# Optimization experiments

Hardware: AMD Instinct MI355X
Metric: run time of the kernel (lower is better)

Reference implementation:

```python
import jax, jax.numpy as jnp
import numpy as np

N_NODES = 100000
N_EDGES = 1600000
IN_DIM = 128
HEADS = 4
OUT_DIM = 32
NEG_SLOPE = 0.2  # PyG GATConv default negative_slope


def setup_inputs() -> dict:
    key = jax.random.key(0)
    k_x, k_e, k_w, k_as, k_ad = jax.random.split(key, 5)
    x = jax.random.normal(k_x, (N_NODES, IN_DIM), dtype=jnp.float32)
    edge_index = jax.random.randint(k_e, (2, N_EDGES), 0, N_NODES, dtype=jnp.int64)
    # Glorot-style init for learned parameters (GATConv lin + attention vectors)
    W = jax.random.normal(k_w, (IN_DIM, HEADS * OUT_DIM), dtype=jnp.float32) / np.sqrt(IN_DIM)
    att_src = jax.random.normal(k_as, (HEADS, OUT_DIM), dtype=jnp.float32) / np.sqrt(OUT_DIM)
    att_dst = jax.random.normal(k_ad, (HEADS, OUT_DIM), dtype=jnp.float32) / np.sqrt(OUT_DIM)
    bias = jnp.zeros((HEADS * OUT_DIM,), dtype=jnp.float32)
    return {"x": x, "edge_index": edge_index, "W": W, "att_src": att_src,
            "att_dst": att_dst, "bias": bias}


def reference(x, edge_index, W, att_src, att_dst, bias):
    N = x.shape[0]
    H, D = att_src.shape
    # PyG GATConv default: add self loops
    loop = jnp.arange(N, dtype=edge_index.dtype)
    src = jnp.concatenate([edge_index[0], loop])  # message sources  [E+N]
    dst = jnp.concatenate([edge_index[1], loop])  # message targets  [E+N]

    h = (x @ W).reshape(N, H, D)                          # [N, H, D]
    a_src = jnp.einsum('nhd,hd->nh', h, att_src)          # [N, H]
    a_dst = jnp.einsum('nhd,hd->nh', h, att_dst)          # [N, H]

    # per-edge attention logits, LeakyReLU(neg_slope=0.2)
    e = jax.nn.leaky_relu(a_src[src] + a_dst[dst], NEG_SLOPE)  # [E+N, H]

    # segment softmax over edges grouped by target node (numerically stable)
    e_max = jax.ops.segment_max(e, dst, num_segments=N)        # [N, H]
    e_max = jnp.where(jnp.isfinite(e_max), e_max, jnp.float32(0))
    ex = jnp.exp(e - e_max[dst])                               # [E+N, H]
    denom = jax.ops.segment_sum(ex, dst, num_segments=N)       # [N, H]
    alpha = ex / (denom[dst] + jnp.float32(1e-16))             # [E+N, H]

    # weighted scatter-aggregate of source features
    msg = h[src] * alpha[:, :, None]                           # [E+N, H, D]
    out = jax.ops.segment_sum(msg, dst, num_segments=N)        # [N, H, D]
    out = out.reshape(N, H * D) + bias                         # concat heads + bias
    return jax.nn.elu(out)                                     # wrapper ELU
```

## Files before the change

kernel.cpp:

```cpp
#include <hip/hip_runtime.h>
#include <hip/hip_fp16.h>
#include <math.h>

#define N_NODES 100000
#define N_EDGES 1600000
#define IN_DIM 128
#define F_DIM 128
#define NEG_SLOPE 0.2f

#define BUCKW_LOG 7
#define NBUCK 784
#define NBLK 128
#define EPB 12500
#define G_TOT (NBUCK * NBLK)
#define SC_CHUNK 4096
#define SC_NB ((G_TOT + SC_CHUNK - 1) / SC_CHUNK)
#define CSR_CAP (N_EDGES + NBUCK * 384)

typedef short v8s __attribute__((ext_vector_type(8)));
typedef float v4f __attribute__((ext_vector_type(4)));

static __device__ __forceinline__ unsigned short f2bf(float f) {
    unsigned u = __float_as_uint(f);
    u += 0x7fffu + ((u >> 16) & 1u);
    return (unsigned short)(u >> 16);
}
static __device__ __forceinline__ float bf2f(unsigned s) { return __uint_as_float(s << 16); }
static __device__ __forceinline__ float lo2f(unsigned u) { return __uint_as_float(u << 16); }
static __device__ __forceinline__ float hi2f(unsigned u) { return __uint_as_float(u & 0xffff0000u); }

__global__ __launch_bounds__(256) void k_wprep(const float* __restrict__ W,
                                               unsigned short* __restrict__ Wt) {
    int i = blockIdx.x * 256 + threadIdx.x;
    int n = i >> 7, k = i & 127;
    Wt[n * 128 + k] = f2bf(W[k * 128 + n]);
}

__global__ __launch_bounds__(256) void k_gemm(const float* __restrict__ x,
                                              const unsigned short* __restrict__ Wt,
                                              unsigned short* __restrict__ h16,
                                              const float* __restrict__ att_src,
                                              const float* __restrict__ att_dst,
                                              float* __restrict__ a_src,
                                              float* __restrict__ a_dst) {
    __shared__ unsigned short As[64][136];
    __shared__ unsigned short Bs[128][136];
    __shared__ float attl[256];
    const int t  = threadIdx.x;
    const int n0 = blockIdx.x * 64;

    attl[t] = (t < 128) ? att_src[t] : att_dst[t - 128];

    {
        int row = t >> 2, k0 = (t & 3) * 32;
        int n = n0 + row;
        #pragma unroll
        for (int i = 0; i < 4; i++) {
            float4 va = make_float4(0.f,0.f,0.f,0.f), vb = va;
            if (n < N_NODES) {
                const float* p = x + (size_t)n * IN_DIM + k0 + i * 8;
                va = *(const float4*)p;
                vb = *(const float4*)(p + 4);
            }
            uint4 u;
            u.x = f2bf(va.x) | ((unsigned)f2bf(va.y) << 16);
            u.y = f2bf(va.z) | ((unsigned)f2bf(va.w) << 16);
            u.z = f2bf(vb.x) | ((unsigned)f2bf(vb.y) << 16);
            u.w = f2bf(vb.z) | ((unsigned)f2bf(vb.w) << 16);
            *(uint4*)&As[row][k0 + i * 8] = u;
        }
    }
    {
        int nr = t >> 1, s0 = (t & 1) * 64;
        const uint4* src = (const uint4*)(Wt + nr * 128 + s0);
        #pragma unroll
        for (int i = 0; i < 8; i++)
            *(uint4*)&Bs[nr][s0 + i * 8] = src[i];
    }
    __syncthreads();

    const int w = t >> 6, lane = t & 63;
    const int mr = lane & 15, quad = lane >> 4;
    const int m0 = w * 16;

    v4f acc[8];
    #pragma unroll
    for (int nt = 0; nt < 8; nt++) acc[nt] = (v4f){0.f, 0.f, 0.f, 0.f};

    #pragma unroll
    for (int kk = 0; kk < 4; kk++) {
        int kof = kk * 32 + quad * 8;
        v8s a = *(const v8s*)&As[m0 + mr][kof];
        #pragma unroll
        for (int nt = 0; nt < 8; nt++) {
            v8s b = *(const v8s*)&Bs[nt * 16 + mr][kof];
            acc[nt] = __builtin_amdgcn_mfma_f32_16x16x32_bf16(a, b, acc[nt], 0, 0, 0);
        }
    }

    #pragma unroll
    for (int nt = 0; nt < 8; nt++)
        #pragma unroll
        for (int r = 0; r < 4; r++)
            As[m0 + quad * 4 + r][nt * 16 + mr] = f2bf(acc[nt][r]);
    __syncthreads();
    {
        int row = m0 + (lane >> 2);
        int c0  = (lane & 3) * 32;
        int n = n0 + row;
        if (n < N_NODES) {
            float ds = 0.f, dd = 0.f;
            #pragma unroll
            for (int i = 0; i < 4; i++) {
                uint4 v = *(const uint4*)&As[row][c0 + i * 8];
                *(uint4*)&h16[(size_t)n * F_DIM + c0 + i * 8] = v;
                float f0 = lo2f(v.x), f1 = hi2f(v.x);
                float f2 = lo2f(v.y), f3 = hi2f(v.y);
                float f4 = lo2f(v.z), f5 = hi2f(v.z);
                float f6 = lo2f(v.w), f7 = hi2f(v.w);
                const float* ps = &attl[c0 + i * 8];
                const float* pd = &attl[128 + c0 + i * 8];
                ds += f0*ps[0] + f1*ps[1] + f2*ps[2] + f3*ps[3]
                    + f4*ps[4] + f5*ps[5] + f6*ps[6] + f7*ps[7];
                dd += f0*pd[0] + f1*pd[1] + f2*pd[2] + f3*pd[3]
                    + f4*pd[4] + f5*pd[5] + f6*pd[6] + f7*pd[7];
            }
            int hd = lane & 3;
            a_src[n * 4 + hd] = ds;
            a_dst[n * 4 + hd] = dd;
        }
    }
}

__global__ __launch_bounds__(1024) void k_bhist(const int* __restrict__ ei_dst,
                                                int* __restrict__ G) {
    __shared__ int hist[NBUCK];
    for (int i = threadIdx.x; i < NBUCK; i += 1024) hist[i] = 0;
    __syncthreads();
    const int4* p = (const int4*)(ei_dst + blockIdx.x * EPB);
    const int n4 = EPB / 4;
    for (int i = threadIdx.x; i < n4; i += 1024) {
        int4 d = p[i];
        atomicAdd(&hist[d.x >> BUCKW_LOG], 1);
        atomicAdd(&hist[d.y >> BUCKW_LOG], 1);
        atomicAdd(&hist[d.z >> BUCKW_LOG], 1);
        atomicAdd(&hist[d.w >> BUCKW_LOG], 1);
    }
    __syncthreads();
    for (int b = threadIdx.x; b < NBUCK; b += 1024)
        G[b * NBLK + blockIdx.x] = hist[b];
}

__global__ __launch_bounds__(256) void k_scanp(const int* __restrict__ a,
                                               int* __restrict__ part) {
    int base = blockIdx.x * SC_CHUNK + threadIdx.x * 16;
    int s = 0;
    #pragma unroll
    for (int i = 0; i < 16; i++) {
        int idx = base + i;
        if (idx < G_TOT) s += a[idx];
    }
    __shared__ int wsum[4];
    for (int off = 32; off >= 1; off >>= 1) s += __shfl_down(s, off, 64);
    if ((threadIdx.x & 63) == 0) wsum[threadIdx.x >> 6] = s;
    __syncthreads();
    if (threadIdx.x == 0) part[blockIdx.x] = wsum[0] + wsum[1] + wsum[2] + wsum[3];
}

__global__ void k_scant(int* part, int* boff) {
    int lane = threadIdx.x & 63;
    int v = (lane < SC_NB) ? part[lane] : 0;
    int x = v;
    #pragma unroll
    for (int off = 1; off < 64; off <<= 1) {
        int y = __shfl_up(x, off, 64);
        if (lane >= off) x += y;
    }
    if (lane < SC_NB) part[lane] = x - v;
    if (lane == 0) boff[NBUCK] = N_EDGES;
}

__global__ __launch_bounds__(256) void k_scand(int* __restrict__ a,
                                               const int* __restrict__ part,
                                               int* __restrict__ boff) {
    __shared__ int tsum[256];
    int tid  = threadIdx.x;
    int base = blockIdx.x * SC_CHUNK + tid * 16;
    int v[16]; int s = 0;
    #pragma unroll
    for (int i = 0; i < 16; i++) {
        int idx = base + i;
        v[i] = (idx < G_TOT) ? a[idx] : 0;
        s += v[i];
    }
    tsum[tid] = s;
    __syncthreads();
    for (int off = 1; off < 256; off <<= 1) {
        int y = (tid >= off) ? tsum[tid - off] : 0;
        __syncthreads();
        tsum[tid] += y;
        __syncthreads();
    }
    int run = part[blockIdx.x] + tsum[tid] - s;
    #pragma unroll
    for (int i = 0; i < 16; i++) {
        int idx = base + i;
        if (idx < G_TOT) {
            a[idx] = run;
            if (idx % NBLK == 0) boff[idx / NBLK] = run;
        }
        run += v[i];
    }
}

__global__ __launch_bounds__(1024) void k_bscat(const int* __restrict__ ei,
                                                const int* __restrict__ G,
                                                int* __restrict__ ebuf) {
    __shared__ int base[NBUCK];
    for (int b = threadIdx.x; b < NBUCK; b += 1024)
        base[b] = G[b * NBLK + blockIdx.x];
    __syncthreads();
    const int4* ps = (const int4*)(ei + blockIdx.x * EPB);
    const int4* pd = (const int4*)(ei + N_EDGES + blockIdx.x * EPB);
    const int n4 = EPB / 4;
    for (int i = threadIdx.x; i < n4; i += 1024) {
        int4 s = ps[i];
        int4 d = pd[i];
        int b0 = d.x >> BUCKW_LOG; int p0 = atomicAdd(&base[b0], 1);
        ebuf[p0] = s.x | ((d.x & 127) << 17);
        int b1 = d.y >> BUCKW_LOG; int p1 = atomicAdd(&base[b1], 1);
        ebuf[p1] = s.y | ((d.y & 127) << 17);
        int b2 = d.z >> BUCKW_LOG; int p2 = atomicAdd(&base[b2], 1);
        ebuf[p2] = s.z | ((d.z & 127) << 17);
        int b3 = d.w >> BUCKW_LOG; int p3 = atomicAdd(&base[b3], 1);
        ebuf[p3] = s.w | ((d.w & 127) << 17);
    }
}

__global__ __launch_bounds__(512) void k_csrfin(const int* __restrict__ ebuf,
                                                const int* __restrict__ boff,
                                                const float* __restrict__ a_src,
                                                const float* __restrict__ a_dst,
                                                int2* __restrict__ ebounds,
                                                int* __restrict__ csr2,
                                                __half* __restrict__ pbuf) {
    __shared__ int cnt[128];
    __shared__ int off[128];
    __shared__ int wtot;
    int b = blockIdx.x;
    int beg = boff[b], end = boff[b + 1];
    int padded_base = beg + b * 384;
    int tid = threadIdx.x;
    if (tid < 128) cnt[tid] = 0;
    __syncthreads();
    {
        int j = beg + tid;
        for (; j + 3 * 512 < end; j += 4 * 512) {
            int e0 = ebuf[j];
            int e1 = ebuf[j + 512];
            int e2 = ebuf[j + 1024];
            int e3 = ebuf[j + 1536];
            atomicAdd(&cnt[(e0 >> 17) & 127], 1);
            atomicAdd(&cnt[(e1 >> 17) & 127], 1);
            atomicAdd(&cnt[(e2 >> 17) & 127], 1);
            atomicAdd(&cnt[(e3 >> 17) & 127], 1);
        }
        for (; j < end; j += 512)
            atomicAdd(&cnt[(ebuf[j] >> 17) & 127], 1);
    }
    __syncthreads();
    if (tid < 128) {
        int cp = (cnt[tid] + 3) & ~3;
        int x = cp;
        #pragma unroll
        for (int o = 1; o < 64; o <<= 1) {
            int y = __shfl_up(x, o, 64);
            if ((tid & 63) >= o) x += y;
        }
        off[tid] = x - cp;
        if (tid == 63) wtot = x;
    }
    __syncthreads();
    if (tid < 128) {
        int v = off[tid] + ((tid >= 64) ? wtot : 0) + padded_base;
        off[tid] = v;
        int node = (b << BUCKW_LOG) + tid;
        int c = cnt[tid];
        if (node < N_NODES) {
            ebounds[node] = make_int2(v, v + c);
            int cpad = (c + 3) & ~3;
            for (int k = c; k < cpad; k++) {
                int pos = v + k;
                csr2[pos] = node;
                *(uint2*)&pbuf[(size_t)pos * 4] = make_uint2(0u, 0u);
            }
        }
        cnt[tid] = 0;
    }
    __syncthreads();
    #define PLACE(pv) {                                                        \
        int dl = ((pv) >> 17) & 127;                                           \
        int s  = (pv) & 0x1ffff;                                               \
        int r = atomicAdd(&cnt[dl], 1);                                        \
        int pos = off[dl] + r;                                                 \
        csr2[pos] = s;                                                         \
        int d = (b << BUCKW_LOG) + dl;                                         \
        float4 as = *(const float4*)&a_src[s * 4];                             \
        float4 ad = *(const float4*)&a_dst[d * 4];                             \
        float e0 = as.x + ad.x; e0 = e0 > 0.f ? e0 : NEG_SLOPE * e0;           \
        float e1 = as.y + ad.y; e1 = e1 > 0.f ? e1 : NEG_SLOPE * e1;           \
        float e2 = as.z + ad.z; e2 = e2 > 0.f ? e2 : NEG_SLOPE * e2;           \
        float e3 = as.w + ad.w; e3 = e3 > 0.f ? e3 : NEG_SLOPE * e3;           \
        __half2 lo = __floats2half2_rn(__expf(e0), __expf(e1));                \
        __half2 hi = __floats2half2_rn(__expf(e2), __expf(e3));                \
        *(uint2*)&pbuf[(size_t)pos * 4] =                                      \
            make_uint2(*(unsigned*)&lo, *(unsigned*)&hi);                      \
    }
    {
        int j = beg + tid;
        for (; j + 3 * 512 < end; j += 4 * 512) {
            int e0 = ebuf[j];
            int e1 = ebuf[j + 512];
            int e2 = ebuf[j + 1024];
            int e3 = ebuf[j + 1536];
            PLACE(e0); PLACE(e1); PLACE(e2); PLACE(e3);
        }
        for (; j < end; j += 512) {
            int e0 = ebuf[j];
            PLACE(e0);
        }
    }
    #undef PLACE
}

__global__ __launch_bounds__(256) void k_agg(const uint4* __restrict__ h16x4,
                                             const float* __restrict__ a_src,
                                             const float* __restrict__ a_dst,
                                             const int2* __restrict__ ebounds,
                                             const int* __restrict__ csr2,
                                             const __half* __restrict__ pbuf,
                                             const float* __restrict__ bias,
                                             float* __restrict__ out) {
    int n = (blockIdx.x * 256 + threadIdx.x) >> 6;
    if (n >= N_NODES) return;
    int lane = threadIdx.x & 63;
    int grp = lane >> 4, g = lane & 15, hd = g >> 2;

    float p0 = 0.f;
    if (grp == 0) {
        float e0 = a_src[n * 4 + hd] + a_dst[n * 4 + hd];
        e0 = e0 > 0.f ? e0 : NEG_SLOPE * e0;
        p0 = __expf(e0);
    }
    uint4 hs = h16x4[(size_t)n * 16 + g];
    float l  = p0;
    float a0 = p0 * lo2f(hs.x), a1 = p0 * hi2f(hs.x);
    float a2 = p0 * lo2f(hs.y), a3 = p0 * hi2f(hs.y);
    float a4 = p0 * lo2f(hs.z), a5 = p0 * hi2f(hs.z);
    float a6 = p0 * lo2f(hs.w), a7 = p0 * hi2f(hs.w);

    int2 eb = ebounds[n];
    int beg = eb.x, cnt = eb.y - eb.x;
    const int* sp = csr2 + beg + grp;
    const __half* pp = pbuf + (size_t)(beg + grp) * 4 + hd;
    int steps = (cnt + 3) >> 2;
    int t = 0;
    for (; t + 4 <= steps; t += 4) {
        int s0 = sp[4 * t];
        int s1 = sp[4 * t + 4];
        int s2 = sp[4 * t + 8];
        int s3 = sp[4 * t + 12];
        float q0 = __half2float(pp[16 * t]);
        float q1 = __half2float(pp[16 * t + 16]);
        float q2 = __half2float(pp[16 * t + 32]);
        float q3 = __half2float(pp[16 * t + 48]);
        uint4 h0 = h16x4[(size_t)s0 * 16 + g];
        uint4 h1 = h16x4[(size_t)s1 * 16 + g];
        uint4 h2 = h16x4[(size_t)s2 * 16 + g];
        uint4 h3 = h16x4[(size_t)s3 * 16 + g];
        l  += (q0 + q1) + (q2 + q3);
        a0 += q0 * lo2f(h0.x) + q1 * lo2f(h1.x) + q2 * lo2f(h2.x) + q3 * lo2f(h3.x);
        a1 += q0 * hi2f(h0.x) + q1 * hi2f(h1.x) + q2 * hi2f(h2.x) + q3 * hi2f(h3.x);
        a2 += q0 * lo2f(h0.y) + q1 * lo2f(h1.y) + q2 * lo2f(h2.y) + q3 * lo2f(h3.y);
        a3 += q0 * hi2f(h0.y) + q1 * hi2f(h1.y) + q2 * hi2f(h2.y) + q3 * hi2f(h3.y);
        a4 += q0 * lo2f(h0.z) + q1 * lo2f(h1.z) + q2 * lo2f(h2.z) + q3 * lo2f(h3.z);
        a5 += q0 * hi2f(h0.z) + q1 * hi2f(h1.z) + q2 * hi2f(h2.z) + q3 * hi2f(h3.z);
        a6 += q0 * lo2f(h0.w) + q1 * lo2f(h1.w) + q2 * lo2f(h2.w) + q3 * lo2f(h3.w);
        a7 += q0 * hi2f(h0.w) + q1 * hi2f(h1.w) + q2 * hi2f(h2.w) + q3 * hi2f(h3.w);
    }
    for (; t < steps; ++t) {
        int s0 = sp[4 * t];
        float q0 = __half2float(pp[16 * t]);
        uint4 h0 = h16x4[(size_t)s0 * 16 + g];
        l  += q0;
        a0 += q0 * lo2f(h0.x);
        a1 += q0 * hi2f(h0.x);
        a2 += q0 * lo2f(h0.y);
        a3 += q0 * hi2f(h0.y);
        a4 += q0 * lo2f(h0.z);
        a5 += q0 * hi2f(h0.z);
        a6 += q0 * lo2f(h0.w);
        a7 += q0 * hi2f(h0.w);
    }
    #define RED2(v) v += __shfl_xor(v, 16, 64); v += __shfl_xor(v, 32, 64);
    RED2(l); RED2(a0); RED2(a1); RED2(a2); RED2(a3);
    RED2(a4); RED2(a5); RED2(a6); RED2(a7);
    #undef RED2

    if (grp == 0) {
        float inv = 1.f / (l + 1e-16f);
        float4 b0 = *(const float4*)&bias[g * 8];
        float4 b1 = *(const float4*)&bias[g * 8 + 4];
        float o0 = a0 * inv + b0.x, o1 = a1 * inv + b0.y;
        float o2 = a2 * inv + b0.z, o3 = a3 * inv + b0.w;
        float o4 = a4 * inv + b1.x, o5 = a5 * inv + b1.y;
        float o6 = a6 * inv + b1.z, o7 = a7 * inv + b1.w;
        o0 = o0 > 0.f ? o0 : __expf(o0) - 1.f;
        o1 = o1 > 0.f ? o1 : __expf(o1) - 1.f;
        o2 = o2 > 0.f ? o2 : __expf(o2) - 1.f;
        o3 = o3 > 0.f ? o3 : __expf(o3) - 1.f;
        o4 = o4 > 0.f ? o4 : __expf(o4) - 1.f;
        o5 = o5 > 0.f ? o5 : __expf(o5) - 1.f;
        o6 = o6 > 0.f ? o6 : __expf(o6) - 1.f;
        o7 = o7 > 0.f ? o7 : __expf(o7) - 1.f;
        *(float4*)&out[(size_t)n * F_DIM + g * 8]     = make_float4(o0, o1, o2, o3);
        *(float4*)&out[(size_t)n * F_DIM + g * 8 + 4] = make_float4(o4, o5, o6, o7);
    }
}

extern "C" void kernel_launch(void* const* d_in, const int* in_sizes, int n_in,
                              void* d_out, int out_size, void* d_ws, size_t ws_size,
                              hipStream_t stream) {
    const float* x       = (const float*)d_in[0];
    const int*   ei      = (const int*)d_in[1];
    const float* W       = (const float*)d_in[2];
    const float* att_src = (const float*)d_in[3];
    const float* att_dst = (const float*)d_in[4];
    const float* bias    = (const float*)d_in[5];
    float*       out     = (float*)d_out;

    char* ws = (char*)d_ws;
    unsigned short* h16 = (unsigned short*)ws; ws += (size_t)N_NODES * F_DIM * 2;
    unsigned short* Wt  = (unsigned short*)ws; ws += (size_t)IN_DIM * F_DIM * 2;
    float* a_src  = (float*)ws; ws += (size_t)N_NODES * 4 * 4;
    float* a_dst  = (float*)ws; ws += (size_t)N_NODES * 4 * 4;
    int*   G      = (int*)ws;   ws += (size_t)G_TOT * 4;
    int*   part   = (int*)ws;   ws += 1024;
    int*   boff   = (int*)ws;   ws += 4096;
    int2*  ebounds= (int2*)ws;  ws += (size_t)N_NODES * 8 + 512;
    int*   ebuf   = (int*)ws;   ws += (size_t)N_EDGES * 4;
    int*   csr2   = (int*)ws;   ws += (size_t)CSR_CAP * 4;
    __half* pbuf  = (__half*)ws; ws += (size_t)CSR_CAP * 4 * 2;

    k_wprep<<<64, 256, 0, stream>>>(W, Wt);
    k_gemm<<<(N_NODES + 63) / 64, 256, 0, stream>>>(x, Wt, h16, att_src, att_dst, a_src, a_dst);

    k_bhist<<<NBLK, 1024, 0, stream>>>(ei + N_EDGES, G);
    k_scanp<<<SC_NB, 256, 0, stream>>>(G, part);
    k_scant<<<1, 64, 0, stream>>>(part, boff);
    k_scand<<<SC_NB, 256, 0, stream>>>(G, part, boff);
    k_bscat<<<NBLK, 1024, 0, stream>>>(ei, G, ebuf);
    k_csrfin<<<NBUCK, 512, 0, stream>>>(ebuf, boff, a_src, a_dst, ebounds, csr2, pbuf);

    k_agg<<<(N_NODES * 64 + 255) / 256, 256, 0, stream>>>((const uint4*)h16, a_src, a_dst, ebounds, csr2, pbuf, bias, out);
}
```

Measured before the change: 268.7 us.

## Compute edge attention weights inside aggregation instead of precomputing fp16 buffer

Removes the per-edge exp-weight buffer that the CSR-finalize kernel wrote in fp16. The aggregation kernel now gathers a_src for each source, applies LeakyReLU and exp on the fly, and masks padding entries through a high bit in the CSR index. This drops the write and re-read of the weight buffer and the a_src/a_dst gathers in csrfin. In exchange, each of the four redundant 16-lane groups now does an extra a_src gather and exp per edge, and the main loop is unrolled by two instead of four. Precision also changes slightly because the weights are no longer rounded to fp16.

Result: faster. 255.4 us (-5.0%).

```diff
diff --git a/kernel.cpp b/kernel.cpp
--- a/kernel.cpp
+++ b/kernel.cpp
@@ -16,6 +16,7 @@
 #define SC_CHUNK 4096
 #define SC_NB ((G_TOT + SC_CHUNK - 1) / SC_CHUNK)
 #define CSR_CAP (N_EDGES + NBUCK * 384)
+#define PADBIT 0x80000000u
 
 typedef short v8s __attribute__((ext_vector_type(8)));
 typedef float v4f __attribute__((ext_vector_type(4)));
@@ -25,7 +26,6 @@
     u += 0x7fffu + ((u >> 16) & 1u);
     return (unsigned short)(u >> 16);
 }
-static __device__ __forceinline__ float bf2f(unsigned s) { return __uint_as_float(s << 16); }
 static __device__ __forceinline__ float lo2f(unsigned u) { return __uint_as_float(u << 16); }
 static __device__ __forceinline__ float hi2f(unsigned u) { return __uint_as_float(u & 0xffff0000u); }
 
@@ -239,11 +239,8 @@
 
 __global__ __launch_bounds__(512) void k_csrfin(const int* __restrict__ ebuf,
                                                 const int* __restrict__ boff,
-                                                const float* __restrict__ a_src,
-                                                const float* __restrict__ a_dst,
                                                 int2* __restrict__ ebounds,
-                                                int* __restrict__ csr2,
-                                                __half* __restrict__ pbuf) {
+                                                int* __restrict__ csr2) {
     __shared__ int cnt[128];
     __shared__ int off[128];
     __shared__ int wtot;
@@ -289,33 +286,12 @@
         if (node < N_NODES) {
             ebounds[node] = make_int2(v, v + c);
             int cpad = (c + 3) & ~3;
-            for (int k = c; k < cpad; k++) {
-                int pos = v + k;
-                csr2[pos] = node;
-                *(uint2*)&pbuf[(size_t)pos * 4] = make_uint2(0u, 0u);
-            }
+            for (int k = c; k < cpad; k++)
+                csr2[v + k] = node | PADBIT;
         }
         cnt[tid] = 0;
     }
     __syncthreads();
-    #define PLACE(pv) {                                                        \
-        int dl = ((pv) >> 17) & 127;                                           \
-        int s  = (pv) & 0x1ffff;                                               \
-        int r = atomicAdd(&cnt[dl], 1);                                        \
-        int pos = off[dl] + r;                                                 \
-        csr2[pos] = s;                                                         \
-        int d = (b << BUCKW_LOG) + dl;                                         \
-        float4 as = *(const float4*)&a_src[s * 4];                             \
-        float4 ad = *(const float4*)&a_dst[d * 4];                             \
-        float e0 = as.x + ad.x; e0 = e0 > 0.f ? e0 : NEG_SLOPE * e0;           \
-        float e1 = as.y + ad.y; e1 = e1 > 0.f ? e1 : NEG_SLOPE * e1;           \
-        float e2 = as.z + ad.z; e2 = e2 > 0.f ? e2 : NEG_SLOPE * e2;           \
-        float e3 = as.w + ad.w; e3 = e3 > 0.f ? e3 : NEG_SLOPE * e3;           \
-        __half2 lo = __floats2half2_rn(__expf(e0), __expf(e1));                \
-        __half2 hi = __floats2half2_rn(__expf(e2), __expf(e3));                \
-        *(uint2*)&pbuf[(size_t)pos * 4] =                                      \
-            make_uint2(*(unsigned*)&lo, *(unsigned*)&hi);                      \
-    }
     {
         int j = beg + tid;
         for (; j + 3 * 512 < end; j += 4 * 512) {
@@ -323,14 +299,21 @@
             int e1 = ebuf[j + 512];
             int e2 = ebuf[j + 1024];
             int e3 = ebuf[j + 1536];
-            PLACE(e0); PLACE(e1); PLACE(e2); PLACE(e3);
+            int d0 = (e0 >> 17) & 127; int r0 = atomicAdd(&cnt[d0], 1);
+            csr2[off[d0] + r0] = e0 & 0x1ffff;
+            int d1 = (e1 >> 17) & 127; int r1 = atomicAdd(&cnt[d1], 1);
+            csr2[off[d1] + r1] = e1 & 0x1ffff;
+            int d2 = (e2 >> 17) & 127; int r2 = atomicAdd(&cnt[d2], 1);
+            csr2[off[d2] + r2] = e2 & 0x1ffff;
+            int d3 = (e3 >> 17) & 127; int r3 = atomicAdd(&cnt[d3], 1);
+            csr2[off[d3] + r3] = e3 & 0x1ffff;
         }
         for (; j < end; j += 512) {
             int e0 = ebuf[j];
-            PLACE(e0);
-        }
-    }
-    #undef PLACE
+            int d0 = (e0 >> 17) & 127; int r0 = atomicAdd(&cnt[d0], 1);
+            csr2[off[d0] + r0] = e0 & 0x1ffff;
+        }
+    }
 }
 
 __global__ __launch_bounds__(256) void k_agg(const uint4* __restrict__ h16x4,
@@ -338,7 +321,6 @@
                                              const float* __restrict__ a_dst,
                                              const int2* __restrict__ ebounds,
                                              const int* __restrict__ csr2,
-                                             const __half* __restrict__ pbuf,
                                              const float* __restrict__ bias,
                                              float* __restrict__ out) {
     int n = (blockIdx.x * 256 + threadIdx.x) >> 6;
@@ -346,9 +328,10 @@
     int lane = threadIdx.x & 63;
     int grp = lane >> 4, g = lane & 15, hd = g >> 2;
 
+    float adn = a_dst[n * 4 + hd];
     float p0 = 0.f;
     if (grp == 0) {
-        float e0 = a_src[n * 4 + hd] + a_dst[n * 4 + hd];
+        float e0 = a_src[n * 4 + hd] + adn;
         e0 = e0 > 0.f ? e0 : NEG_SLOPE * e0;
         p0 = __expf(e0);
     }
@@ -362,36 +345,41 @@
     int2 eb = ebounds[n];
     int beg = eb.x, cnt = eb.y - eb.x;
     const int* sp = csr2 + beg + grp;
-    const __half* pp = pbuf + (size_t)(beg + grp) * 4 + hd;
     int steps = (cnt + 3) >> 2;
     int t = 0;
-    for (; t + 4 <= steps; t += 4) {
-        int s0 = sp[4 * t];
-        int s1 = sp[4 * t + 4];
-        int s2 = sp[4 * t + 8];
-        int s3 = sp[4 * t + 12];
-        float q0 = __half2float(pp[16 * t]);
-        float q1 = __half2float(pp[16 * t + 16]);
-        float q2 = __half2float(pp[16 * t + 32]);
-        float q3 = __half2float(pp[16 * t + 48]);
+    for (; t + 2 <= steps; t += 2) {
+        int u0 = sp[4 * t];
+        int u1 = sp[4 * t + 4];
+        int s0 = u0 & 0x7fffffff;
+        int s1 = u1 & 0x7fffffff;
+        float w0 = a_src[s0 * 4 + hd] + adn;
+        float w1 = a_src[s1 * 4 + hd] + adn;
         uint4 h0 = h16x4[(size_t)s0 * 16 + g];
         uint4 h1 = h16x4[(size_t)s1 * 16 + g];
-        uint4 h2 = h16x4[(size_t)s2 * 16 + g];
-        uint4 h3 = h16x4[(size_t)s3 * 16 + g];
-        l  += (q0 + q1) + (q2 + q3);
-        a0 += q0 * lo2f(h0.x) + q1 * lo2f(h1.x) + q2 * lo2f(h2.x) + q3 * lo2f(h3.x);
-        a1 += q0 * hi2f(h0.x) + q1 * hi2f(h1.x) + q2 * hi2f(h2.x) + q3 * hi2f(h3.x);
-        a2 += q0 * lo2f(h0.y) + q1 * lo2f(h1.y) + q2 * lo2f(h2.y) + q3 * lo2f(h3.y);
-        a3 += q0 * hi2f(h0.y) + q1 * hi2f(h1.y) + q2 * hi2f(h2.y) + q3 * hi2f(h3.y);
-        a4 += q0 * lo2f(h0.z) + q1 * lo2f(h1.z) + q2 * lo2f(h2.z) + q3 * lo2f(h3.z);
-        a5 += q0 * hi2f(h0.z) + q1 * hi2f(h1.z) + q2 * hi2f(h2.z) + q3 * hi2f(h3.z);
-        a6 += q0 * lo2f(h0.w) + q1 * lo2f(h1.w) + q2 * lo2f(h2.w) + q3 * lo2f(h3.w);
-        a7 += q0 * hi2f(h0.w) + q1 * hi2f(h1.w) + q2 * hi2f(h2.w) + q3 * hi2f(h3.w);
-    }
-    for (; t < steps; ++t) {
-        int s0 = sp[4 * t];
-        float q0 = __half2float(pp[16 * t]);
+        w0 = w0 > 0.f ? w0 : NEG_SLOPE * w0;
+        w1 = w1 > 0.f ? w1 : NEG_SLOPE * w1;
+        float q0 = __expf(w0);
+        float q1 = __expf(w1);
+        q0 = u0 < 0 ? 0.f : q0;
+        q1 = u1 < 0 ? 0.f : q1;
+        l  += q0 + q1;
+        a0 += q0 * lo2f(h0.x) + q1 * lo2f(h1.x);
+        a1 += q0 * hi2f(h0.x) + q1 * hi2f(h1.x);
+        a2 += q0 * lo2f(h0.y) + q1 * lo2f(h1.y);
+        a3 += q0 * hi2f(h0.y) + q1 * hi2f(h1.y);
+        a4 += q0 * lo2f(h0.z) + q1 * lo2f(h1.z);
+        a5 += q0 * hi2f(h0.z) + q1 * hi2f(h1.z);
+        a6 += q0 * lo2f(h0.w) + q1 * lo2f(h1.w);
+        a7 += q0 * hi2f(h0.w) + q1 * hi2f(h1.w);
+    }
+    if (t < steps) {
+        int u0 = sp[4 * t];
+        int s0 = u0 & 0x7fffffff;
+        float w0 = a_src[s0 * 4 + hd] + adn;
         uint4 h0 = h16x4[(size_t)s0 * 16 + g];
+        w0 = w0 > 0.f ? w0 : NEG_SLOPE * w0;
+        float q0 = __expf(w0);
+        q0 = u0 < 0 ? 0.f : q0;
         l  += q0;
         a0 += q0 * lo2f(h0.x);
         a1 += q0 * hi2f(h0.x);
@@ -450,7 +438,6 @@
     int2*  ebounds= (int2*)ws;  ws += (size_t)N_NODES * 8 + 512;
     int*   ebuf   = (int*)ws;   ws += (size_t)N_EDGES * 4;
     int*   csr2   = (int*)ws;   ws += (size_t)CSR_CAP * 4;
-    __half* pbuf  = (__half*)ws; ws += (size_t)CSR_CAP * 4 * 2;
 
     k_wprep<<<64, 256, 0, stream>>>(W, Wt);
     k_gemm<<<(N_NODES + 63) / 64, 256, 0, stream>>>(x, Wt, h16, att_src, att_dst, a_src, a_dst);
@@ -460,7 +447,7 @@
     k_scant<<<1, 64, 0, stream>>>(part, boff);
     k_scand<<<SC_NB, 256, 0, stream>>>(G, part, boff);
     k_bscat<<<NBLK, 1024, 0, stream>>>(ei, G, ebuf);
-    k_csrfin<<<NBUCK, 512, 0, stream>>>(ebuf, boff, a_src, a_dst, ebounds, csr2, pbuf);
-
-    k_agg<<<(N_NODES * 64 + 255) / 256, 256, 0, stream>>>((const uint4*)h16, a_src, a_dst, ebounds, csr2, pbuf, bias, out);
-}
+    k_csrfin<<<NBUCK, 512, 0, stream>>>(ebuf, boff, ebounds, csr2);
+
+    k_agg<<<(N_NODES * 64 + 255) / 256, 256, 0, stream>>>((const uint4*)h16, a_src, a_dst, ebounds, csr2, bias, out);
+}
```
